# Performance work log

Hardware: AMD Instinct MI355X
Metric: run time of the kernel (lower is better)

## Reference

```python
import jax, jax.numpy as jnp
import numpy as np

N = 50000      # nodes
E = 800000     # edges (avg degree 16)
F_IN = 128
H = 4          # heads
F_OUT = 64


def setup_inputs() -> dict:
    key = jax.random.key(0)
    ks = jax.random.split(key, 10)
    feat = jax.random.normal(ks[0], (N, F_IN), jnp.float32)
    src = jax.random.randint(ks[1], (E,), 0, N, dtype=jnp.int32)
    dst = jax.random.randint(ks[2], (E,), 0, N, dtype=jnp.int32)
    # fc: Linear(F_IN -> H*F_OUT, bias=False); torch weight layout [H*F_OUT, F_IN]
    fc_w = jax.random.normal(ks[3], (H * F_OUT, F_IN), jnp.float32) * (1.0 / np.sqrt(F_IN))
    # attention vectors live in input-feature space: (1, H, F_IN) -> store as (H, F_IN)
    attn_l = jax.random.normal(ks[4], (H, F_IN), jnp.float32) * 0.1
    attn_r = jax.random.normal(ks[5], (H, F_IN), jnp.float32) * 0.1
    attn_l1 = jax.random.normal(ks[6], (H, F_IN), jnp.float32) * 0.1
    attn_r1 = jax.random.normal(ks[7], (H, F_IN), jnp.float32) * 0.1
    bias = jax.random.normal(ks[8], (H * F_OUT,), jnp.float32) * 0.01
    return {"feat": feat, "src": src, "dst": dst, "fc_w": fc_w,
            "attn_l": attn_l, "attn_r": attn_r,
            "attn_l1": attn_l1, "attn_r1": attn_r1, "bias": bias}


def reference(feat, src, dst, fc_w, attn_l, attn_r, attn_l1, attn_r1, bias):
    n = feat.shape[0]
    h, f_out = attn_l.shape[0], fc_w.shape[0] // attn_l.shape[0]

    fs = feat[src]  # [E, F_in] gather
    fd = feat[dst]  # [E, F_in] gather

    # e1[e,h] = sum_f (feat[src]*attn_l)[h,f] * (feat[dst]*attn_r)[h,f]
    e1 = jnp.einsum('ef,ef,hf->eh', fs, fd, attn_l * attn_r)
    # e2 same with attn_l1/attn_r1
    e2 = jnp.einsum('ef,ef,hf->eh', fs, fd, attn_l1 * attn_r1)
    # e3 = ||feat[src]*attn_l1||^2 + ||feat[dst]*attn_r1||^2 (per node, then gathered)
    el2 = jnp.einsum('nf,hf->nh', feat * feat, attn_l1 * attn_l1)  # [N, H]
    er2 = jnp.einsum('nf,hf->nh', feat * feat, attn_r1 * attn_r1)  # [N, H]

    e = e1 - 2.0 * e2 + el2[src] + er2[dst]  # [E, H] squared-distance score

    # edge_softmax: softmax over incoming edges of each destination node
    m = jax.ops.segment_max(e, dst, num_segments=n)          # [N, H]
    ex = jnp.exp(e - m[dst])                                  # [E, H]
    denom = jax.ops.segment_sum(ex, dst, num_segments=n)     # [N, H]
    a = ex / denom[dst]                                       # [E, H]

    # feature projection then u_mul_e + sum aggregation
    ft = (feat @ fc_w.T).reshape(n, h, f_out)                 # [N, H, F_out]
    rst = jax.ops.segment_sum(ft[src] * a[:, :, None], dst, num_segments=n)

    return rst + bias.reshape(1, h, f_out)
```

## Files before the change

kernel.cpp:

```cpp
#include <hip/hip_runtime.h>

#define N_NODES 50000
#define N_EDGES 800000
#define F_IN    128
#define NH      4
#define C_OUT   256
#define CAP     64

typedef short bf16x8 __attribute__((ext_vector_type(8)));
typedef float f32x4  __attribute__((ext_vector_type(4)));

__device__ __forceinline__ unsigned short f2bf(float f) {
    union { float f; unsigned int u; } v; v.f = f;
    return (unsigned short)((v.u + 0x7FFFu + ((v.u >> 16) & 1u)) >> 16);
}
__device__ __forceinline__ float asf(unsigned u) { union { unsigned u; float f; } v; v.u = u; return v.f; }

__device__ __forceinline__ void unp8(uint4 u, float* f) {
    f[0] = asf(u.x << 16); f[1] = asf(u.x & 0xffff0000u);
    f[2] = asf(u.y << 16); f[3] = asf(u.y & 0xffff0000u);
    f[4] = asf(u.z << 16); f[5] = asf(u.z & 0xffff0000u);
    f[6] = asf(u.w << 16); f[7] = asf(u.w & 0xffff0000u);
}

__global__ __launch_bounds__(256) void k_cvt(const float* __restrict__ feat,
                                             const float* __restrict__ fcw,
                                             unsigned short* __restrict__ fb16,
                                             unsigned short* __restrict__ wb16,
                                             int* __restrict__ deg) {
    int i = blockIdx.x * 256 + threadIdx.x;
    const int NF = N_NODES * F_IN / 4;
    const int NW = C_OUT * F_IN / 4;
    if (i < N_NODES) deg[i] = 0;
    if (i < NF) {
        float4 v = ((const float4*)feat)[i];
        ushort4 o = { f2bf(v.x), f2bf(v.y), f2bf(v.z), f2bf(v.w) };
        ((ushort4*)fb16)[i] = o;
    } else if (i < NF + NW) {
        int j = i - NF;
        float4 v = ((const float4*)fcw)[j];
        ushort4 o = { f2bf(v.x), f2bf(v.y), f2bf(v.z), f2bf(v.w) };
        ((ushort4*)wb16)[j] = o;
    }
}

__global__ void k_scatter(const int* __restrict__ src, const int* __restrict__ dst,
                          int* __restrict__ deg, int* __restrict__ esrc) {
    int e = blockIdx.x * 256 + threadIdx.x;
    if (e >= N_EDGES) return;
    int d = dst[e];
    int pos = atomicAdd(&deg[d], 1);
    if (pos < CAP)
        esrc[(size_t)d * CAP + pos] = src[e];
}

__global__ __launch_bounds__(256) void k_fused(const unsigned short* __restrict__ fb16,
                                               const unsigned short* __restrict__ wb16,
                                               const float* __restrict__ al, const float* __restrict__ ar,
                                               const float* __restrict__ al1, const float* __restrict__ ar1,
                                               const int* __restrict__ esrc,
                                               const int* __restrict__ degv,
                                               const float* __restrict__ bias,
                                               float* __restrict__ out) {
    __shared__ float s_w2[512];
    __shared__ float s_wl2[512];
    __shared__ float s_bias[256];
    __shared__ unsigned short s_af[16 * 136];

    int t = threadIdx.x;
    for (int i = t; i < 512; i += 256) {
        s_w2[i]  = al[i] * ar[i] - 2.0f * al1[i] * ar1[i];
        s_wl2[i] = al1[i] * al1[i];
    }
    s_bias[t] = bias[t];
    __syncthreads();

    int w = t >> 6, l = t & 63, h = l & 3, cb = l >> 2;
    int d = blockIdx.x * 4 + w;
    int deg = degv[d];
    const int* ep = esrc + (size_t)d * CAP;

    float w2[8], wl2[8], fd[8], tt[8];
#pragma unroll
    for (int j = 0; j < 8; ++j) {
        w2[j]  = s_w2[h * 128 + cb * 8 + j];
        wl2[j] = s_wl2[h * 128 + cb * 8 + j];
    }
    uint4 ud = ((const uint4*)fb16)[(size_t)d * 16 + cb];
    unp8(ud, fd);
#pragma unroll
    for (int j = 0; j < 8; ++j) tt[j] = fd[j] * w2[j];

    float m = -3.4e38f, den = 0.f;
    float acc[8] = {0.f, 0.f, 0.f, 0.f, 0.f, 0.f, 0.f, 0.f};

    for (int j0 = 0; j0 < deg; j0 += 4) {
        int4 i4 = *(const int4*)(ep + j0);
        int idx[4] = { i4.x, i4.y, i4.z, i4.w };
#pragma unroll
        for (int k = 1; k < 4; ++k)
            if (j0 + k >= deg) idx[k] = i4.x;
        uint4 u[4];
#pragma unroll
        for (int k = 0; k < 4; ++k)
            u[k] = ((const uint4*)fb16)[(size_t)idx[k] * 16 + cb];
        float fs[4][8], s[4];
#pragma unroll
        for (int k = 0; k < 4; ++k) {
            unp8(u[k], fs[k]);
            float p = 0.f;
#pragma unroll
            for (int j = 0; j < 8; ++j) {
                float v1 = fmaf(fs[k][j], wl2[j], tt[j]);
                p = fmaf(fs[k][j], v1, p);
            }
#pragma unroll
            for (int mk = 4; mk < 64; mk <<= 1)
                p += __shfl_xor(p, mk, 64);
            s[k] = p;
        }
        float mb = fmaxf(fmaxf(s[0], s[1]), fmaxf(s[2], s[3]));
        float mn = fmaxf(m, mb);
        float sc = __expf(m - mn);
        den *= sc;
#pragma unroll
        for (int j = 0; j < 8; ++j) acc[j] *= sc;
#pragma unroll
        for (int k = 0; k < 4; ++k) {
            float ex = (j0 + k < deg) ? __expf(s[k] - mn) : 0.f;
            den += ex;
#pragma unroll
            for (int j = 0; j < 8; ++j) acc[j] = fmaf(ex, fs[k][j], acc[j]);
        }
        m = mn;
    }

    float inv = (den > 0.f) ? 1.0f / den : 0.f;
    {
        unsigned o0 = ((unsigned)f2bf(acc[1] * inv) << 16) | f2bf(acc[0] * inv);
        unsigned o1 = ((unsigned)f2bf(acc[3] * inv) << 16) | f2bf(acc[2] * inv);
        unsigned o2 = ((unsigned)f2bf(acc[5] * inv) << 16) | f2bf(acc[4] * inv);
        unsigned o3 = ((unsigned)f2bf(acc[7] * inv) << 16) | f2bf(acc[6] * inv);
        *(uint4*)&s_af[(w * 4 + h) * 136 + cb * 8] = make_uint4(o0, o1, o2, o3);
    }
    __syncthreads();

    int n = l & 15, q = l >> 4;
    bf16x8 afr[4];
#pragma unroll
    for (int step = 0; step < 4; ++step)
        afr[step] = *(const bf16x8*)&s_af[n * 136 + step * 32 + q * 8];

    f32x4 c[4] = {};
#pragma unroll
    for (int h4 = 0; h4 < 4; ++h4) {
#pragma unroll
        for (int step = 0; step < 4; ++step) {
            union { uint4 u; bf16x8 v; } b;
            b.u = *(const uint4*)(wb16 + (size_t)(h4 * 64 + w * 16 + n) * 128 + step * 32 + q * 8);
            c[h4] = __builtin_amdgcn_mfma_f32_16x16x32_bf16(afr[step], b.v, c[h4], 0, 0, 0);
        }
    }
    int node = blockIdx.x * 4 + q;
#pragma unroll
    for (int h4 = 0; h4 < 4; ++h4)
        out[(size_t)node * 256 + h4 * 64 + w * 16 + n] = c[h4][h4] + s_bias[h4 * 64 + w * 16 + n];
}

extern "C" void kernel_launch(void* const* d_in, const int* in_sizes, int n_in,
                              void* d_out, int out_size, void* d_ws, size_t ws_size,
                              hipStream_t stream) {
    const float* feat = (const float*)d_in[0];
    const int*   src  = (const int*)d_in[1];
    const int*   dst  = (const int*)d_in[2];
    const float* fcw  = (const float*)d_in[3];
    const float* al   = (const float*)d_in[4];
    const float* ar   = (const float*)d_in[5];
    const float* al1  = (const float*)d_in[6];
    const float* ar1  = (const float*)d_in[7];
    const float* bias = (const float*)d_in[8];
    float* out = (float*)d_out;

    char* ws = (char*)d_ws;
    size_t o = 0;
    auto take = [&](size_t b) -> void* {
        void* p = ws + o;
        o = (o + b + 255) & ~(size_t)255;
        return p;
    };
    unsigned short* fb16 = (unsigned short*)take((size_t)N_NODES * F_IN * 2);
    unsigned short* wb16 = (unsigned short*)take((size_t)C_OUT * F_IN * 2);
    int* esrc = (int*)take((size_t)N_NODES * CAP * 4);
    int* deg  = (int*)take((size_t)N_NODES * 4);

    const int CVT_T = N_NODES * F_IN / 4 + C_OUT * F_IN / 4;
    k_cvt<<<(CVT_T + 255) / 256, 256, 0, stream>>>(feat, fcw, fb16, wb16, deg);
    k_scatter<<<(N_EDGES + 255) / 256, 256, 0, stream>>>(src, dst, deg, esrc);
    k_fused<<<N_NODES / 4, 256, 0, stream>>>(fb16, wb16, al, ar, al1, ar1, esrc, deg, bias, out);
}
```

Measured before the change: 301.4 us.

## Gather fp32 features directly with double-buffered prefetch and fold conversion into scatter

Drops the bf16 feature conversion pass and has the fused kernel gather fp32 neighbor rows directly. The weight conversion is merged into the edge scatter kernel, and the degree array is zeroed with a memset. The edge loop is software-pipelined with two register buffers so the next four neighbor rows load while the current ones are processed. This removes one full pass over the features and overlaps gather latency with compute, at the cost of twice the gather bytes and more registers per thread.

```diff
diff --git a/kernel.cpp b/kernel.cpp
--- a/kernel.cpp
+++ b/kernel.cpp
@@ -6,6 +6,8 @@
 #define NH      4
 #define C_OUT   256
 #define CAP     64
+#define EDGE_BLOCKS 3125
+#define W_BLOCKS    32
 
 typedef short bf16x8 __attribute__((ext_vector_type(8)));
 typedef float f32x4  __attribute__((ext_vector_type(4)));
@@ -14,47 +16,31 @@
     union { float f; unsigned int u; } v; v.f = f;
     return (unsigned short)((v.u + 0x7FFFu + ((v.u >> 16) & 1u)) >> 16);
 }
-__device__ __forceinline__ float asf(unsigned u) { union { unsigned u; float f; } v; v.u = u; return v.f; }
-
-__device__ __forceinline__ void unp8(uint4 u, float* f) {
-    f[0] = asf(u.x << 16); f[1] = asf(u.x & 0xffff0000u);
-    f[2] = asf(u.y << 16); f[3] = asf(u.y & 0xffff0000u);
-    f[4] = asf(u.z << 16); f[5] = asf(u.z & 0xffff0000u);
-    f[6] = asf(u.w << 16); f[7] = asf(u.w & 0xffff0000u);
-}
-
-__global__ __launch_bounds__(256) void k_cvt(const float* __restrict__ feat,
-                                             const float* __restrict__ fcw,
-                                             unsigned short* __restrict__ fb16,
-                                             unsigned short* __restrict__ wb16,
-                                             int* __restrict__ deg) {
-    int i = blockIdx.x * 256 + threadIdx.x;
-    const int NF = N_NODES * F_IN / 4;
-    const int NW = C_OUT * F_IN / 4;
-    if (i < N_NODES) deg[i] = 0;
-    if (i < NF) {
-        float4 v = ((const float4*)feat)[i];
-        ushort4 o = { f2bf(v.x), f2bf(v.y), f2bf(v.z), f2bf(v.w) };
-        ((ushort4*)fb16)[i] = o;
-    } else if (i < NF + NW) {
-        int j = i - NF;
-        float4 v = ((const float4*)fcw)[j];
-        ushort4 o = { f2bf(v.x), f2bf(v.y), f2bf(v.z), f2bf(v.w) };
-        ((ushort4*)wb16)[j] = o;
-    }
-}
-
-__global__ void k_scatter(const int* __restrict__ src, const int* __restrict__ dst,
-                          int* __restrict__ deg, int* __restrict__ esrc) {
-    int e = blockIdx.x * 256 + threadIdx.x;
-    if (e >= N_EDGES) return;
-    int d = dst[e];
-    int pos = atomicAdd(&deg[d], 1);
-    if (pos < CAP)
-        esrc[(size_t)d * CAP + pos] = src[e];
-}
-
-__global__ __launch_bounds__(256) void k_fused(const unsigned short* __restrict__ fb16,
+
+__global__ __launch_bounds__(256) void k_prep(const float* __restrict__ fcw,
+                                              unsigned short* __restrict__ wb16,
+                                              const int* __restrict__ src,
+                                              const int* __restrict__ dst,
+                                              int* __restrict__ deg,
+                                              int* __restrict__ esrc) {
+    int bid = blockIdx.x;
+    if (bid < EDGE_BLOCKS) {
+        int e = bid * 256 + threadIdx.x;
+        int d = dst[e];
+        int pos = atomicAdd(&deg[d], 1);
+        if (pos < CAP)
+            esrc[(size_t)d * CAP + pos] = src[e];
+    } else {
+        int j = (bid - EDGE_BLOCKS) * 256 + threadIdx.x;
+        if (j < C_OUT * F_IN / 4) {
+            float4 v = ((const float4*)fcw)[j];
+            ushort4 o = { f2bf(v.x), f2bf(v.y), f2bf(v.z), f2bf(v.w) };
+            ((ushort4*)wb16)[j] = o;
+        }
+    }
+}
+
+__global__ __launch_bounds__(256) void k_fused(const float* __restrict__ feat,
                                                const unsigned short* __restrict__ wb16,
                                                const float* __restrict__ al, const float* __restrict__ ar,
                                                const float* __restrict__ al1, const float* __restrict__ ar1,
@@ -76,48 +62,55 @@
     __syncthreads();
 
     int w = t >> 6, l = t & 63, h = l & 3, cb = l >> 2;
-    int d = blockIdx.x * 4 + w;
+    int d = __builtin_amdgcn_readfirstlane(blockIdx.x * 4 + w);
     int deg = degv[d];
+    if (deg > CAP) deg = CAP;
     const int* ep = esrc + (size_t)d * CAP;
 
-    float w2[8], wl2[8], fd[8], tt[8];
-#pragma unroll
-    for (int j = 0; j < 8; ++j) {
-        w2[j]  = s_w2[h * 128 + cb * 8 + j];
-        wl2[j] = s_wl2[h * 128 + cb * 8 + j];
-    }
-    uint4 ud = ((const uint4*)fb16)[(size_t)d * 16 + cb];
-    unp8(ud, fd);
-#pragma unroll
-    for (int j = 0; j < 8; ++j) tt[j] = fd[j] * w2[j];
+    float wl2[8], tt[8];
+    {
+        float4 q0 = ((const float4*)(feat + (size_t)d * F_IN + cb * 8))[0];
+        float4 q1 = ((const float4*)(feat + (size_t)d * F_IN + cb * 8))[1];
+        float fd[8] = { q0.x, q0.y, q0.z, q0.w, q1.x, q1.y, q1.z, q1.w };
+#pragma unroll
+        for (int j = 0; j < 8; ++j) {
+            float w2 = s_w2[h * 128 + cb * 8 + j];
+            wl2[j]   = s_wl2[h * 128 + cb * 8 + j];
+            tt[j]    = fd[j] * w2;
+        }
+    }
 
     float m = -3.4e38f, den = 0.f;
     float acc[8] = {0.f, 0.f, 0.f, 0.f, 0.f, 0.f, 0.f, 0.f};
 
-    for (int j0 = 0; j0 < deg; j0 += 4) {
-        int4 i4 = *(const int4*)(ep + j0);
-        int idx[4] = { i4.x, i4.y, i4.z, i4.w };
-#pragma unroll
-        for (int k = 1; k < 4; ++k)
-            if (j0 + k >= deg) idx[k] = i4.x;
-        uint4 u[4];
-#pragma unroll
-        for (int k = 0; k < 4; ++k)
-            u[k] = ((const uint4*)fb16)[(size_t)idx[k] * 16 + cb];
-        float fs[4][8], s[4];
+    auto prefetch = [&](int j, float (&dstv)[4][8]) {
+        int4 i4 = *(const int4*)(ep + j);
+        int id[4] = { i4.x, i4.y, i4.z, i4.w };
 #pragma unroll
         for (int k = 0; k < 4; ++k) {
-            unp8(u[k], fs[k]);
+            unsigned v = (unsigned)id[k];
+            if (v >= N_NODES) v = 0;
+            const float4* rp = (const float4*)(feat + (size_t)v * F_IN + cb * 8);
+            float4 a = rp[0], b = rp[1];
+            dstv[k][0] = a.x; dstv[k][1] = a.y; dstv[k][2] = a.z; dstv[k][3] = a.w;
+            dstv[k][4] = b.x; dstv[k][5] = b.y; dstv[k][6] = b.z; dstv[k][7] = b.w;
+        }
+    };
+
+    auto compute = [&](int j0, float (&cur)[4][8]) {
+        float s[4];
+#pragma unroll
+        for (int k = 0; k < 4; ++k) {
             float p = 0.f;
 #pragma unroll
             for (int j = 0; j < 8; ++j) {
-                float v1 = fmaf(fs[k][j], wl2[j], tt[j]);
-                p = fmaf(fs[k][j], v1, p);
+                float v1 = fmaf(cur[k][j], wl2[j], tt[j]);
+                p = fmaf(cur[k][j], v1, p);
             }
 #pragma unroll
             for (int mk = 4; mk < 64; mk <<= 1)
                 p += __shfl_xor(p, mk, 64);
-            s[k] = p;
+            s[k] = (j0 + k < deg) ? p : -3.4e38f;
         }
         float mb = fmaxf(fmaxf(s[0], s[1]), fmaxf(s[2], s[3]));
         float mn = fmaxf(m, mb);
@@ -130,9 +123,22 @@
             float ex = (j0 + k < deg) ? __expf(s[k] - mn) : 0.f;
             den += ex;
 #pragma unroll
-            for (int j = 0; j < 8; ++j) acc[j] = fmaf(ex, fs[k][j], acc[j]);
+            for (int j = 0; j < 8; ++j) acc[j] = fmaf(ex, cur[k][j], acc[j]);
         }
         m = mn;
+    };
+
+    if (deg > 0) {
+        float A0[4][8], A1[4][8];
+        prefetch(0, A0);
+        for (int j0 = 0; j0 < deg; j0 += 8) {
+            prefetch(j0 + 4, A1);
+            compute(j0, A0);
+            if (j0 + 4 < deg) {
+                prefetch(j0 + 8, A0);
+                compute(j0 + 4, A1);
+            }
+        }
     }
 
     float inv = (den > 0.f) ? 1.0f / den : 0.f;
@@ -188,13 +194,11 @@
         o = (o + b + 255) & ~(size_t)255;
         return p;
     };
-    unsigned short* fb16 = (unsigned short*)take((size_t)N_NODES * F_IN * 2);
     unsigned short* wb16 = (unsigned short*)take((size_t)C_OUT * F_IN * 2);
     int* esrc = (int*)take((size_t)N_NODES * CAP * 4);
     int* deg  = (int*)take((size_t)N_NODES * 4);
 
-    const int CVT_T = N_NODES * F_IN / 4 + C_OUT * F_IN / 4;
-    k_cvt<<<(CVT_T + 255) / 256, 256, 0, stream>>>(feat, fcw, fb16, wb16, deg);
-    k_scatter<<<(N_EDGES + 255) / 256, 256, 0, stream>>>(src, dst, deg, esrc);
-    k_fused<<<N_NODES / 4, 256, 0, stream>>>(fb16, wb16, al, ar, al1, ar1, esrc, deg, bias, out);
-}
+    hipMemsetAsync(deg, 0, (size_t)N_NODES * 4, stream);
+    k_prep<<<EDGE_BLOCKS + W_BLOCKS, 256, 0, stream>>>(fcw, wb16, src, dst, deg, esrc);
+    k_fused<<<N_NODES / 4, 256, 0, stream>>>(feat, wb16, al, ar, al1, ar1, esrc, deg, bias, out);
+}
```

Result: slower. 319.6 us (+6.0%).

## Compute edge scores and aggregation with MFMA over 16-edge chunks, merge prep kernels

Applied to the files above, without the earlier changes.

The per-lane scalar dot products and shuffle reductions for edge scores are replaced by a bf16 MFMA. Gathered source features are multiplied against a per-destination weighted feature fragment, with the per-node squared-norm term precomputed into an el2 table. Softmax-weighted aggregation also moves to MFMA: gathered rows are staged in LDS and multiplied by the bf16 probabilities, processing 16 edges per iteration instead of 4. The conversion, edge-bucketing and norm precompute are merged into one prep kernel after a memset. This cuts launch count and ALU/shuffle work, but rounds the probabilities to bf16 and adds LDS traffic and per-chunk padding work for low-degree nodes.

```diff
diff --git a/kernel.cpp b/kernel.cpp
--- a/kernel.cpp
+++ b/kernel.cpp
@@ -1,21 +1,21 @@
 #include <hip/hip_runtime.h>
 
 #define N_NODES 50000
-#define N_EDGES 800000
 #define F_IN    128
-#define NH      4
+#define CAP     64
 #define C_OUT   256
-#define CAP     64
+#define EDGE_BLOCKS 3125
+#define W_BLOCKS    32
+#define NODE_BLOCKS 12500
 
 typedef short bf16x8 __attribute__((ext_vector_type(8)));
 typedef float f32x4  __attribute__((ext_vector_type(4)));
 
 __device__ __forceinline__ unsigned short f2bf(float f) {
-    union { float f; unsigned int u; } v; v.f = f;
+    union { float f; unsigned u; } v; v.f = f;
     return (unsigned short)((v.u + 0x7FFFu + ((v.u >> 16) & 1u)) >> 16);
 }
 __device__ __forceinline__ float asf(unsigned u) { union { unsigned u; float f; } v; v.u = u; return v.f; }
-
 __device__ __forceinline__ void unp8(uint4 u, float* f) {
     f[0] = asf(u.x << 16); f[1] = asf(u.x & 0xffff0000u);
     f[2] = asf(u.y << 16); f[3] = asf(u.y & 0xffff0000u);
@@ -23,35 +23,55 @@
     f[6] = asf(u.w << 16); f[7] = asf(u.w & 0xffff0000u);
 }
 
-__global__ __launch_bounds__(256) void k_cvt(const float* __restrict__ feat,
-                                             const float* __restrict__ fcw,
-                                             unsigned short* __restrict__ fb16,
-                                             unsigned short* __restrict__ wb16,
-                                             int* __restrict__ deg) {
-    int i = blockIdx.x * 256 + threadIdx.x;
-    const int NF = N_NODES * F_IN / 4;
-    const int NW = C_OUT * F_IN / 4;
-    if (i < N_NODES) deg[i] = 0;
-    if (i < NF) {
-        float4 v = ((const float4*)feat)[i];
-        ushort4 o = { f2bf(v.x), f2bf(v.y), f2bf(v.z), f2bf(v.w) };
-        ((ushort4*)fb16)[i] = o;
-    } else if (i < NF + NW) {
-        int j = i - NF;
+__global__ __launch_bounds__(256) void k_prep(const float* __restrict__ feat,
+                                              const float* __restrict__ fcw,
+                                              const float* __restrict__ al1,
+                                              const int* __restrict__ src,
+                                              const int* __restrict__ dst,
+                                              int* __restrict__ deg,
+                                              int* __restrict__ esrc,
+                                              unsigned short* __restrict__ fb16,
+                                              unsigned short* __restrict__ wb16,
+                                              float* __restrict__ el2) {
+    int bid = blockIdx.x, t = threadIdx.x;
+    if (bid < EDGE_BLOCKS) {
+        int e = bid * 256 + t;
+        int d = dst[e];
+        int pos = atomicAdd(&deg[d], 1);
+        if (pos < CAP) esrc[(size_t)d * CAP + pos] = src[e];
+    } else if (bid < EDGE_BLOCKS + W_BLOCKS) {
+        int j = (bid - EDGE_BLOCKS) * 256 + t;
         float4 v = ((const float4*)fcw)[j];
         ushort4 o = { f2bf(v.x), f2bf(v.y), f2bf(v.z), f2bf(v.w) };
         ((ushort4*)wb16)[j] = o;
-    }
-}
-
-__global__ void k_scatter(const int* __restrict__ src, const int* __restrict__ dst,
-                          int* __restrict__ deg, int* __restrict__ esrc) {
-    int e = blockIdx.x * 256 + threadIdx.x;
-    if (e >= N_EDGES) return;
-    int d = dst[e];
-    int pos = atomicAdd(&deg[d], 1);
-    if (pos < CAP)
-        esrc[(size_t)d * CAP + pos] = src[e];
+    } else {
+        int r = (bid - EDGE_BLOCKS - W_BLOCKS) * 4 + (t >> 6);
+        int l = t & 63, h = l & 3, cb = l >> 2;
+        const float4* fr = (const float4*)(feat + (size_t)r * F_IN + cb * 8);
+        float4 f0 = fr[0], f1 = fr[1];
+        const float4* ap = (const float4*)(al1 + h * F_IN + cb * 8);
+        float4 a0 = ap[0], a1 = ap[1];
+        float p = 0.f;
+        p = fmaf(f0.x * f0.x, a0.x * a0.x, p);
+        p = fmaf(f0.y * f0.y, a0.y * a0.y, p);
+        p = fmaf(f0.z * f0.z, a0.z * a0.z, p);
+        p = fmaf(f0.w * f0.w, a0.w * a0.w, p);
+        p = fmaf(f1.x * f1.x, a1.x * a1.x, p);
+        p = fmaf(f1.y * f1.y, a1.y * a1.y, p);
+        p = fmaf(f1.z * f1.z, a1.z * a1.z, p);
+        p = fmaf(f1.w * f1.w, a1.w * a1.w, p);
+#pragma unroll
+        for (int o = 4; o < 64; o <<= 1) p += __shfl_xor(p, o, 64);
+        if (cb == 0) el2[r * 4 + h] = p;
+        if (h == 0) {
+            uint4 o4;
+            o4.x = (unsigned)f2bf(f0.x) | ((unsigned)f2bf(f0.y) << 16);
+            o4.y = (unsigned)f2bf(f0.z) | ((unsigned)f2bf(f0.w) << 16);
+            o4.z = (unsigned)f2bf(f1.x) | ((unsigned)f2bf(f1.y) << 16);
+            o4.w = (unsigned)f2bf(f1.z) | ((unsigned)f2bf(f1.w) << 16);
+            ((uint4*)fb16)[(size_t)r * 16 + cb] = o4;
+        }
+    }
 }
 
 __global__ __launch_bounds__(256) void k_fused(const unsigned short* __restrict__ fb16,
@@ -60,111 +80,150 @@
                                                const float* __restrict__ al1, const float* __restrict__ ar1,
                                                const int* __restrict__ esrc,
                                                const int* __restrict__ degv,
+                                               const float* __restrict__ el2,
                                                const float* __restrict__ bias,
                                                float* __restrict__ out) {
     __shared__ float s_w2[512];
-    __shared__ float s_wl2[512];
     __shared__ float s_bias[256];
     __shared__ unsigned short s_af[16 * 136];
+    __shared__ unsigned short s_fs[4][16 * 136];
 
     int t = threadIdx.x;
-    for (int i = t; i < 512; i += 256) {
-        s_w2[i]  = al[i] * ar[i] - 2.0f * al1[i] * ar1[i];
-        s_wl2[i] = al1[i] * al1[i];
-    }
+    for (int i = t; i < 512; i += 256)
+        s_w2[i] = al[i] * ar[i] - 2.0f * al1[i] * ar1[i];
     s_bias[t] = bias[t];
     __syncthreads();
 
-    int w = t >> 6, l = t & 63, h = l & 3, cb = l >> 2;
-    int d = blockIdx.x * 4 + w;
-    int deg = degv[d];
-    const int* ep = esrc + (size_t)d * CAP;
-
-    float w2[8], wl2[8], fd[8], tt[8];
-#pragma unroll
-    for (int j = 0; j < 8; ++j) {
-        w2[j]  = s_w2[h * 128 + cb * 8 + j];
-        wl2[j] = s_wl2[h * 128 + cb * 8 + j];
-    }
-    uint4 ud = ((const uint4*)fb16)[(size_t)d * 16 + cb];
-    unp8(ud, fd);
-#pragma unroll
-    for (int j = 0; j < 8; ++j) tt[j] = fd[j] * w2[j];
+    int w = t >> 6, l = t & 63, g = l >> 4, ecol = l & 15;
+    int d = __builtin_amdgcn_readfirstlane(blockIdx.x * 4 + w);
+    int deg = degv[d]; if (deg > CAP) deg = CAP;
+    const int* ep = esrc + d * CAP;
+
+    uint4 wfr[4];
+    {
+        int hc = ecol & 3;
+        bool hv = ecol < 4;
+#pragma unroll
+        for (int s = 0; s < 4; ++s) {
+            uint4 u = ((const uint4*)fb16)[d * 16 + s * 4 + g];
+            float fd[8]; unp8(u, fd);
+            int k0 = s * 32 + g * 8;
+            float wv[8];
+#pragma unroll
+            for (int j = 0; j < 8; ++j)
+                wv[j] = hv ? fd[j] * s_w2[hc * 128 + k0 + j] : 0.f;
+            uint4 o;
+            o.x = (unsigned)f2bf(wv[0]) | ((unsigned)f2bf(wv[1]) << 16);
+            o.y = (unsigned)f2bf(wv[2]) | ((unsigned)f2bf(wv[3]) << 16);
+            o.z = (unsigned)f2bf(wv[4]) | ((unsigned)f2bf(wv[5]) << 16);
+            o.w = (unsigned)f2bf(wv[6]) | ((unsigned)f2bf(wv[7]) << 16);
+            wfr[s] = o;
+        }
+    }
 
     float m = -3.4e38f, den = 0.f;
-    float acc[8] = {0.f, 0.f, 0.f, 0.f, 0.f, 0.f, 0.f, 0.f};
-
-    for (int j0 = 0; j0 < deg; j0 += 4) {
-        int4 i4 = *(const int4*)(ep + j0);
-        int idx[4] = { i4.x, i4.y, i4.z, i4.w };
-#pragma unroll
-        for (int k = 1; k < 4; ++k)
-            if (j0 + k >= deg) idx[k] = i4.x;
-        uint4 u[4];
-#pragma unroll
-        for (int k = 0; k < 4; ++k)
-            u[k] = ((const uint4*)fb16)[(size_t)idx[k] * 16 + cb];
-        float fs[4][8], s[4];
-#pragma unroll
-        for (int k = 0; k < 4; ++k) {
-            unp8(u[k], fs[k]);
-            float p = 0.f;
-#pragma unroll
-            for (int j = 0; j < 8; ++j) {
-                float v1 = fmaf(fs[k][j], wl2[j], tt[j]);
-                p = fmaf(fs[k][j], v1, p);
-            }
-#pragma unroll
-            for (int mk = 4; mk < 64; mk <<= 1)
-                p += __shfl_xor(p, mk, 64);
-            s[k] = p;
-        }
-        float mb = fmaxf(fmaxf(s[0], s[1]), fmaxf(s[2], s[3]));
-        float mn = fmaxf(m, mb);
-        float sc = __expf(m - mn);
-        den *= sc;
-#pragma unroll
-        for (int j = 0; j < 8; ++j) acc[j] *= sc;
-#pragma unroll
-        for (int k = 0; k < 4; ++k) {
-            float ex = (j0 + k < deg) ? __expf(s[k] - mn) : 0.f;
-            den += ex;
-#pragma unroll
-            for (int j = 0; j < 8; ++j) acc[j] = fmaf(ex, fs[k][j], acc[j]);
-        }
+    f32x4 acc[8];
+#pragma unroll
+    for (int b = 0; b < 8; ++b) acc[b] = (f32x4){0.f, 0.f, 0.f, 0.f};
+
+    for (int c0 = 0; c0 < deg; c0 += 16) {
+        int4 i4 = *(const int4*)(ep + c0 + g * 4);
+        unsigned er = (unsigned)ep[c0 + ecol];
+        if (er >= N_NODES) er = 0;
+        unsigned ce[4] = { (unsigned)i4.x, (unsigned)i4.y, (unsigned)i4.z, (unsigned)i4.w };
+#pragma unroll
+        for (int r = 0; r < 4; ++r) if (ce[r] >= N_NODES) ce[r] = 0;
+
+        f32x4 sc;
+#pragma unroll
+        for (int r = 0; r < 4; ++r) sc[r] = el2[ce[r] * 4 + (ecol & 3)];
+
+        uint4 fsr[4];
+#pragma unroll
+        for (int s = 0; s < 4; ++s)
+            fsr[s] = ((const uint4*)fb16)[er * 16u + s * 4 + g];
+
+#pragma unroll
+        for (int s = 0; s < 4; ++s) {
+            union { uint4 u; bf16x8 v; } a, b;
+            a.u = fsr[s]; b.u = wfr[s];
+            sc = __builtin_amdgcn_mfma_f32_16x16x32_bf16(a.v, b.v, sc, 0, 0, 0);
+        }
+
+#pragma unroll
+        for (int s = 0; s < 4; ++s)
+            *(uint4*)&s_fs[w][ecol * 136 + s * 32 + g * 8] = fsr[s];
+
+        float s4[4];
+#pragma unroll
+        for (int r = 0; r < 4; ++r)
+            s4[r] = (c0 + g * 4 + r < deg) ? sc[r] : -3.4e38f;
+        float mx = fmaxf(fmaxf(s4[0], s4[1]), fmaxf(s4[2], s4[3]));
+        mx = fmaxf(mx, __shfl_xor(mx, 16, 64));
+        mx = fmaxf(mx, __shfl_xor(mx, 32, 64));
+        float mn = fmaxf(m, mx);
+        float rs = __expf(m - mn);
+        den *= rs;
+#pragma unroll
+        for (int b = 0; b < 8; ++b) {
+            acc[b][0] *= rs; acc[b][1] *= rs; acc[b][2] *= rs; acc[b][3] *= rs;
+        }
+        float p4[4], ps = 0.f;
+#pragma unroll
+        for (int r = 0; r < 4; ++r) { p4[r] = __expf(s4[r] - mn); ps += p4[r]; }
+        ps += __shfl_xor(ps, 16, 64);
+        ps += __shfl_xor(ps, 32, 64);
+        den += ps;
         m = mn;
+
+        union { uint4 u; bf16x8 v; } pf;
+        pf.u.x = f2bf(p4[0]); pf.u.y = f2bf(p4[1]);
+        pf.u.z = f2bf(p4[2]); pf.u.w = f2bf(p4[3]);
+
+        __builtin_amdgcn_wave_barrier();
+#pragma unroll
+        for (int b = 0; b < 8; ++b) {
+            union { uint4 u; bf16x8 v; } af;
+            af.u.x = s_fs[w][(g * 4 + 0) * 136 + b * 16 + ecol];
+            af.u.y = s_fs[w][(g * 4 + 1) * 136 + b * 16 + ecol];
+            af.u.z = s_fs[w][(g * 4 + 2) * 136 + b * 16 + ecol];
+            af.u.w = s_fs[w][(g * 4 + 3) * 136 + b * 16 + ecol];
+            acc[b] = __builtin_amdgcn_mfma_f32_16x16x32_bf16(af.v, pf.v, acc[b], 0, 0, 0);
+        }
+        __builtin_amdgcn_wave_barrier();
     }
 
     float inv = (den > 0.f) ? 1.0f / den : 0.f;
-    {
-        unsigned o0 = ((unsigned)f2bf(acc[1] * inv) << 16) | f2bf(acc[0] * inv);
-        unsigned o1 = ((unsigned)f2bf(acc[3] * inv) << 16) | f2bf(acc[2] * inv);
-        unsigned o2 = ((unsigned)f2bf(acc[5] * inv) << 16) | f2bf(acc[4] * inv);
-        unsigned o3 = ((unsigned)f2bf(acc[7] * inv) << 16) | f2bf(acc[6] * inv);
-        *(uint4*)&s_af[(w * 4 + h) * 136 + cb * 8] = make_uint4(o0, o1, o2, o3);
+    if (ecol < 4) {
+        int row = w * 4 + ecol;
+#pragma unroll
+        for (int b = 0; b < 8; ++b) {
+            unsigned lo = (unsigned)f2bf(acc[b][0] * inv) | ((unsigned)f2bf(acc[b][1] * inv) << 16);
+            unsigned hi = (unsigned)f2bf(acc[b][2] * inv) | ((unsigned)f2bf(acc[b][3] * inv) << 16);
+            uint2 o; o.x = lo; o.y = hi;
+            *(uint2*)&s_af[row * 136 + b * 16 + g * 4] = o;
+        }
     }
     __syncthreads();
 
-    int n = l & 15, q = l >> 4;
     bf16x8 afr[4];
 #pragma unroll
     for (int step = 0; step < 4; ++step)
-        afr[step] = *(const bf16x8*)&s_af[n * 136 + step * 32 + q * 8];
-
+        afr[step] = *(const bf16x8*)&s_af[ecol * 136 + step * 32 + g * 8];
     f32x4 c[4] = {};
 #pragma unroll
     for (int h4 = 0; h4 < 4; ++h4) {
 #pragma unroll
         for (int step = 0; step < 4; ++step) {
             union { uint4 u; bf16x8 v; } b;
-            b.u = *(const uint4*)(wb16 + (size_t)(h4 * 64 + w * 16 + n) * 128 + step * 32 + q * 8);
+            b.u = *(const uint4*)(wb16 + (size_t)(h4 * 64 + w * 16 + ecol) * 128 + step * 32 + g * 8);
             c[h4] = __builtin_amdgcn_mfma_f32_16x16x32_bf16(afr[step], b.v, c[h4], 0, 0, 0);
         }
     }
-    int node = blockIdx.x * 4 + q;
+    int node = blockIdx.x * 4 + g;
 #pragma unroll
     for (int h4 = 0; h4 < 4; ++h4)
-        out[(size_t)node * 256 + h4 * 64 + w * 16 + n] = c[h4][h4] + s_bias[h4 * 64 + w * 16 + n];
+        out[(size_t)node * 256 + h4 * 64 + w * 16 + ecol] = c[h4][h4] + s_bias[h4 * 64 + w * 16 + ecol];
 }
 
 extern "C" void kernel_launch(void* const* d_in, const int* in_sizes, int n_in,
@@ -188,13 +247,15 @@
         o = (o + b + 255) & ~(size_t)255;
         return p;
     };
+    unsigned short* wb16 = (unsigned short*)take((size_t)C_OUT * F_IN * 2);
     unsigned short* fb16 = (unsigned short*)take((size_t)N_NODES * F_IN * 2);
-    unsigned short* wb16 = (unsigned short*)take((size_t)C_OUT * F_IN * 2);
-    int* esrc = (int*)take((size_t)N_NODES * CAP * 4);
-    int* deg  = (int*)take((size_t)N_NODES * 4);
-
-    const int CVT_T = N_NODES * F_IN / 4 + C_OUT * F_IN / 4;
-    k_cvt<<<(CVT_T + 255) / 256, 256, 0, stream>>>(feat, fcw, fb16, wb16, deg);
-    k_scatter<<<(N_EDGES + 255) / 256, 256, 0, stream>>>(src, dst, deg, esrc);
-    k_fused<<<N_NODES / 4, 256, 0, stream>>>(fb16, wb16, al, ar, al1, ar1, esrc, deg, bias, out);
-}
+    int*   esrc = (int*)take((size_t)N_NODES * CAP * 4);
+    int*   deg  = (int*)take((size_t)N_NODES * 4);
+    float* el2  = (float*)take((size_t)N_NODES * 4 * 4);
+
+    hipMemsetAsync(deg, 0, (size_t)N_NODES * 4, stream);
+    k_prep<<<EDGE_BLOCKS + W_BLOCKS + NODE_BLOCKS, 256, 0, stream>>>(
+        feat, fcw, al1, src, dst, deg, esrc, fb16, wb16, el2);
+    k_fused<<<N_NODES / 4, 256, 0, stream>>>(
+        fb16, wb16, al, ar, al1, ar1, esrc, deg, el2, bias, out);
+}
```

After: 318.9 us. 1.06x slower.
